# Kernel optimization log

Hardware: AMD Instinct MI355X
Metric: run time of the kernel (lower is better)

Reference implementation:

```python
import jax, jax.numpy as jnp
import numpy as np

BLOCK = 64
EPS = 1e-6
N_HEADS = 16


def _rope(t, cos, sin):
    # t: (B,S,H,hd); cos/sin: (S, hd//2) -> broadcast (1,S,1,hd//2)
    B, S, H, hd = t.shape
    tr = t.reshape(B, S, H, hd // 2, 2)
    t0, t1 = tr[..., 0], tr[..., 1]
    c = cos[None, :, None, :]
    s = sin[None, :, None, :]
    o0 = t0 * c - t1 * s
    o1 = t0 * s + t1 * c
    return jnp.stack([o0, o1], axis=-1).reshape(B, S, H, hd)


def setup_inputs() -> dict:
    key = jax.random.key(0)
    ks = jax.random.split(key, 6)
    B, S, D = 1, 2048, 2048
    hd = D // N_HEADS
    x = jax.random.normal(ks[0], (B, S, D), dtype=jnp.float32)
    # rotary table: theta_i = 10000^(-2i/hd)
    inv_freq = 1.0 / (10000.0 ** (jnp.arange(0, hd, 2, dtype=jnp.float32) / hd))
    t = jnp.arange(S, dtype=jnp.float32)
    freqs = jnp.outer(t, inv_freq)  # (S, hd//2)
    freqs_cos = jnp.cos(freqs)
    freqs_sin = jnp.sin(freqs)
    std = 0.02
    Wq = jax.random.normal(ks[1], (D, D), dtype=jnp.float32) * std
    Wk = jax.random.normal(ks[2], (D, D), dtype=jnp.float32) * std
    Wv = jax.random.normal(ks[3], (D, D), dtype=jnp.float32) * std
    Wo = jax.random.normal(ks[4], (D, D), dtype=jnp.float32) * std
    mask = jnp.ones((1, 1), dtype=bool)  # non-None mask => no masking in original code
    return {"x": x, "freqs_cos": freqs_cos, "freqs_sin": freqs_sin,
            "Wq": Wq, "Wk": Wk, "Wv": Wv, "Wo": Wo, "mask": mask}


def reference(x, freqs_cos, freqs_sin, Wq, Wk, Wv, Wo, mask):
    B, S, D = x.shape
    H = N_HEADS
    hd = D // H
    scale = hd ** -0.5
    nb = S // BLOCK

    q = (x @ Wq.T).reshape(B, S, H, hd)
    k = (x @ Wk.T).reshape(B, S, H, hd)
    v = (x @ Wv.T).reshape(B, S, H, hd)
    q = _rope(q, freqs_cos, freqs_sin)
    k = _rope(k, freqs_cos, freqs_sin)

    # block views: (B, nb, BLOCK, H, hd)
    qb = q.reshape(B, nb, BLOCK, H, hd)
    kb = k.reshape(B, nb, BLOCK, H, hd)
    vb = v.reshape(B, nb, BLOCK, H, hd)

    # per-(i,j) block scores: (B, nb_i, nb_j, H, BLOCK_q, BLOCK_k)
    s = jnp.einsum('binhd,bjmhd->bijhnm', qb, kb) * scale
    # NOTE: original module (mask is not None path) applies NO causal mask and
    # uses the per-block local max (no running-max rescale) -- reproduced exactly.
    m = jnp.max(s, axis=-1, keepdims=True)
    p = jnp.exp(s - m)
    # denominator: sum of per-block row sums over all j blocks -> (B, nb, H, BLOCK)
    L = p.sum(axis=-1).sum(axis=2)
    # numerator: sum over j blocks of p @ v -> (B, nb, BLOCK, H, hd)
    O = jnp.einsum('bijhnm,bjmhd->binhd', p, vb).reshape(B, S, H, hd)
    Lr = L.transpose(0, 1, 3, 2).reshape(B, S, H, 1)  # (B,S,H,1)
    O = O / (Lr + EPS)
    return O.reshape(B, S, D) @ Wo.T
```

## Files before the change

kernel.cpp:

```cpp
#include <hip/hip_runtime.h>
#include <hip/hip_bf16.h>
#include <math.h>

#define SEQ 2048
#define DM  2048
#define NH  16
#define HD  128
#define SCALE 0.08838834764831845f

typedef __bf16 bf16_t;
typedef __bf16 bf16x8 __attribute__((ext_vector_type(8)));
typedef __bf16 bf16x4 __attribute__((ext_vector_type(4)));
typedef float  f32x4  __attribute__((ext_vector_type(4)));
typedef int    i32x4  __attribute__((ext_vector_type(4)));

typedef const __attribute__((address_space(1))) void* gas_ptr;
typedef __attribute__((address_space(3))) void* las_ptr;

__device__ __forceinline__ void gload_lds16(const void* g, void* l) {
    __builtin_amdgcn_global_load_lds((gas_ptr)g, (las_ptr)l, 16, 0, 0);
}

__device__ __forceinline__ f32x4 mfma_bf16(bf16x8 a, bf16x8 b, f32x4 c) {
    return __builtin_amdgcn_mfma_f32_16x16x32_bf16(a, b, c, 0, 0, 0);
}

__device__ __forceinline__ unsigned cvtpk_bf16(float lo, float hi) {
    unsigned d;
    asm("v_cvt_pk_bf16_f32 %0, %1, %2" : "=v"(d) : "v"(lo), "v"(hi));
    return d;
}

__device__ __forceinline__ bf16x8 read_frag64(const bf16_t* lds, int row, int k) {
    int chunk = (k >> 3) ^ (row & 7);
    return *(const bf16x8*)(lds + row * 64 + chunk * 8);
}
__device__ __forceinline__ bf16x8 read_frag128(const bf16_t* lds, int row, int k) {
    int chunk = k >> 3;
    chunk = (chunk & 8) | ((chunk ^ row) & 7);
    return *(const bf16x8*)(lds + row * 128 + chunk * 8);
}
__device__ __forceinline__ bf16x8 read_slab(const bf16_t* sl, int row, int g) {
    int j = g ^ ((row >> 1) & 3);
    return *(const bf16x8*)(sl + row * 32 + j * 8);
}

__global__ __launch_bounds__(256) void cvt5(
    const float* __restrict__ s0, const float* __restrict__ s1,
    const float* __restrict__ s2, const float* __restrict__ s3,
    const float* __restrict__ s4,
    bf16_t* __restrict__ d0, bf16_t* __restrict__ d1, bf16_t* __restrict__ d2,
    bf16_t* __restrict__ d3, bf16_t* __restrict__ d4)
{
    int which = blockIdx.y;
    const float* s; bf16_t* d;
    switch (which) {
        case 0: s = s0; d = d0; break;
        case 1: s = s1; d = d1; break;
        case 2: s = s2; d = d2; break;
        case 3: s = s3; d = d3; break;
        default: s = s4; d = d4; break;
    }
    size_t idx = ((size_t)blockIdx.x * 256 + threadIdx.x) * 4;
    float4 v = *(const float4*)(s + idx);
    bf16x4 o = { (bf16_t)v.x, (bf16_t)v.y, (bf16_t)v.z, (bf16_t)v.w };
    *(bf16x4*)(d + idx) = o;
}

#define BARX() asm volatile("s_barrier" ::: "memory")
#define VMW8 asm volatile("s_waitcnt vmcnt(8)" ::: "memory")
#define VMW4 asm volatile("s_waitcnt vmcnt(4)" ::: "memory")
#define VMW0 asm volatile("s_waitcnt vmcnt(0)" ::: "memory")
#define NOGATE

__global__ __launch_bounds__(512, 2) void qkv_pipe(
    const bf16_t* __restrict__ A,
    const bf16_t* __restrict__ B0, const bf16_t* __restrict__ B1,
    const bf16_t* __restrict__ B2,
    bf16_t* __restrict__ Oq, bf16_t* __restrict__ Ok, bf16_t* __restrict__ Ov,
    const float* __restrict__ fcos, const float* __restrict__ fsin)
{
    __shared__ bf16_t lds[65536];

    const int tid = threadIdx.x;
    const int lane = tid & 63;
    const int w = tid >> 6;
    const int wm = w >> 2;
    const int wn = w & 3;
    const int g4 = lane >> 4, r15 = lane & 15;

    const int bm = blockIdx.y;
    const int bny = blockIdx.x;
    const int sel = bny >> 3;
    const int bnl = bny & 7;
    const bf16_t* Bp = (sel == 0) ? B0 : (sel == 1) ? B1 : B2;

    const size_t arow0 = (size_t)bm * 256;
    const size_t brow0 = (size_t)bnl * 256;

    const int row0 = tid >> 2;
    const int kj0  = (tid & 3) ^ ((row0 >> 1) & 3);
    const bf16_t* pA = A  + (arow0 + row0) * DM + kj0 * 8;
    const bf16_t* pB = Bp + (brow0 + row0) * DM + kj0 * 8;
    char* ldsb = (char*)lds;
    const int off0 = tid * 16;
    const int off1 = 8192 + tid * 16;

    #define STAGE_HT(S) do { if ((S) < 128) {                                   \
        const int T_ = (S) >> 2, a_ = (S) & 3;                                  \
        const int ko_ = T_ * 64 + ((a_ >> 1) << 5);                             \
        char* dst_ = ldsb + (((T_ & 1) << 16) | ((a_ & 1) << 15) | ((a_ >> 1) << 14)); \
        const bf16_t* s0_ = (a_ & 1) ? pB : pA;                                 \
        gload_lds16(s0_ + ko_, dst_ + off0);                                    \
        gload_lds16(s0_ + 128 * DM + ko_, dst_ + off1);                         \
    } } while (0)

    const bf16_t* b0A0 = lds;
    const bf16_t* b0A1 = lds + 8192;
    const bf16_t* b0B0 = lds + 16384;
    const bf16_t* b0B1 = lds + 24576;
    const bf16_t* b1A0 = lds + 32768;
    const bf16_t* b1A1 = lds + 40960;
    const bf16_t* b1B0 = lds + 49152;
    const bf16_t* b1B1 = lds + 57344;

    f32x4 acc[8][4] = {};

    #define PHASE(ASL, BSL, MH, SIDX, GATE, READB)                              \
    {                                                                           \
        _Pragma("unroll")                                                       \
        for (int m = 0; m < 4; ++m)                                             \
            af[m] = read_slab((ASL), wm * 128 + (MH) * 64 + m * 16 + r15, g4);  \
        if (READB) {                                                            \
            _Pragma("unroll")                                                   \
            for (int n = 0; n < 4; ++n)                                         \
                bfr[n] = read_slab((BSL), wn * 64 + n * 16 + r15, g4);          \
        }                                                                       \
        STAGE_HT(SIDX);                                                         \
        GATE;                                                                   \
        BARX();                                                                 \
        __builtin_amdgcn_s_setprio(1);                                          \
        _Pragma("unroll")                                                       \
        for (int m = 0; m < 4; ++m)                                             \
            _Pragma("unroll")                                                   \
            for (int n = 0; n < 4; ++n)                                         \
                acc[(MH) * 4 + m][n] = mfma_bf16(af[m], bfr[n], acc[(MH) * 4 + m][n]); \
        __builtin_amdgcn_s_setprio(0);                                          \
        BARX();                                                                 \
    }

    STAGE_HT(0); STAGE_HT(1); STAGE_HT(2); STAGE_HT(3); STAGE_HT(4); STAGE_HT(5);
    VMW8;
    BARX();

    for (int i = 0; i < 15; ++i) {
        const int s0 = 6 + i * 8;
        bf16x8 af[4], bfr[4];
        PHASE(b0A0, b0B0, 0, s0 + 0, NOGATE, 1)
        PHASE(b0A0, b0B0, 1, s0 + 1, VMW8,   0)
        PHASE(b0A1, b0B1, 0, s0 + 2, NOGATE, 1)
        PHASE(b0A1, b0B1, 1, s0 + 3, VMW8,   0)
        PHASE(b1A0, b1B0, 0, s0 + 4, NOGATE, 1)
        PHASE(b1A0, b1B0, 1, s0 + 5, VMW8,   0)
        PHASE(b1A1, b1B1, 0, s0 + 6, NOGATE, 1)
        PHASE(b1A1, b1B1, 1, s0 + 7, VMW8,   0)
    }
    {
        const int s0 = 6 + 15 * 8;
        bf16x8 af[4], bfr[4];
        PHASE(b0A0, b0B0, 0, s0 + 0, NOGATE, 1)
        PHASE(b0A0, b0B0, 1, s0 + 1, VMW8,   0)
        PHASE(b0A1, b0B1, 0, s0 + 2, NOGATE, 1)
        PHASE(b0A1, b0B1, 1, s0 + 3, VMW4,   0)
        PHASE(b1A0, b1B0, 0, s0 + 4, NOGATE, 1)
        PHASE(b1A0, b1B0, 1, s0 + 5, VMW0,   0)
        PHASE(b1A1, b1B1, 0, s0 + 6, NOGATE, 1)
        PHASE(b1A1, b1B1, 1, s0 + 7, NOGATE, 0)
    }
    #undef PHASE
    #undef STAGE_HT

    const int r0 = bm * 256 + wm * 128;
    const int c0 = bnl * 256 + wn * 64;

    if (sel == 2) {
        #pragma unroll
        for (int m = 0; m < 8; ++m) {
            int rowb = r0 + m * 16 + g4 * 4;
            #pragma unroll
            for (int n = 0; n < 4; ++n) {
                int col = c0 + n * 16 + r15;
                bf16x4 pk = { (bf16_t)acc[m][n][0], (bf16_t)acc[m][n][1],
                              (bf16_t)acc[m][n][2], (bf16_t)acc[m][n][3] };
                *(bf16x4*)&Ov[(size_t)col * SEQ + rowb] = pk;
            }
        }
    } else {
        bf16_t* dst = (sel == 0) ? Oq : Ok;
        #pragma unroll
        for (int m = 0; m < 8; ++m) {
            int rowb = r0 + m * 16 + g4 * 4;
            #pragma unroll
            for (int n = 0; n < 4; ++n) {
                int col = c0 + n * 16 + r15;
                int f = (col & (HD - 1)) >> 1;
                float sgn = (col & 1) ? 1.0f : -1.0f;
                #pragma unroll
                for (int r = 0; r < 4; ++r) {
                    float mine = acc[m][n][r];
                    float other = __shfl_xor(mine, 1);
                    float cc = fcos[(rowb + r) * (HD / 2) + f];
                    float ss = fsin[(rowb + r) * (HD / 2) + f];
                    float o = mine * cc + sgn * other * ss;
                    dst[(size_t)(rowb + r) * DM + col] = (bf16_t)o;
                }
            }
        }
    }
}

__global__ __launch_bounds__(256) void gemm_fin(
    const bf16_t* __restrict__ A, const bf16_t* __restrict__ B0,
    float* __restrict__ Of)
{
    __shared__ bf16_t lA[128 * 64];
    __shared__ bf16_t lB[64 * 64];

    const int tid = threadIdx.x;
    const int lane = tid & 63;
    const int w = tid >> 6;
    const int wm = w >> 1, wn = w & 1;
    const int g = lane >> 4, r15 = lane & 15;

    const int bm = blockIdx.x;
    const int bn = blockIdx.y;

    f32x4 acc[4][2] = {};

    const size_t arow0 = (size_t)bm * 128;
    const size_t brow0 = (size_t)bn * 64;

    for (int kt = 0; kt < DM / 64; ++kt) {
        const int k0 = kt * 64;
        #pragma unroll
        for (int i = 0; i < 4; ++i) {
            int c = i * 256 + tid;
            int row = c >> 3;
            int ck = (c ^ row) & 7;
            const bf16_t* ga = A + (arow0 + row) * DM + k0 + ck * 8;
            gload_lds16(ga, (char*)lA + (i * 256 + w * 64) * 16);
        }
        #pragma unroll
        for (int i = 0; i < 2; ++i) {
            int c = i * 256 + tid;
            int row = c >> 3;
            int ck = (c ^ row) & 7;
            const bf16_t* gb = B0 + (brow0 + row) * DM + k0 + ck * 8;
            gload_lds16(gb, (char*)lB + (i * 256 + w * 64) * 16);
        }
        __syncthreads();
        #pragma unroll
        for (int kk = 0; kk < 2; ++kk) {
            bf16x8 af[4], bfr[2];
            #pragma unroll
            for (int m = 0; m < 4; ++m)
                af[m] = read_frag64(lA, wm * 64 + m * 16 + r15, kk * 32 + g * 8);
            #pragma unroll
            for (int n = 0; n < 2; ++n)
                bfr[n] = read_frag64(lB, wn * 32 + n * 16 + r15, kk * 32 + g * 8);
            #pragma unroll
            for (int m = 0; m < 4; ++m)
                #pragma unroll
                for (int n = 0; n < 2; ++n)
                    acc[m][n] = mfma_bf16(af[m], bfr[n], acc[m][n]);
        }
        __syncthreads();
    }

    const int r0 = bm * 128 + wm * 64;
    const int c0 = bn * 64 + wn * 32;
    #pragma unroll
    for (int m = 0; m < 4; ++m) {
        int rowb = r0 + m * 16 + g * 4;
        #pragma unroll
        for (int n = 0; n < 2; ++n) {
            int col = c0 + n * 16 + r15;
            #pragma unroll
            for (int r = 0; r < 4; ++r)
                Of[(size_t)(rowb + r) * DM + col] = acc[m][n][r];
        }
    }
}

__global__ __launch_bounds__(512, 2) void attn_k6(
    const bf16_t* __restrict__ Q, const bf16_t* __restrict__ Kb,
    const bf16_t* __restrict__ Vt, bf16_t* __restrict__ Op,
    float* __restrict__ Lp)
{
    __shared__ bf16_t lk[2 * 64 * 128];
    __shared__ bf16_t lv[2 * 128 * 64];

    const int tid = threadIdx.x;
    const int lane = tid & 63;
    const int w = tid >> 6;
    const int g = lane >> 4, r15 = lane & 15;
    const int qb = blockIdx.x;
    const int h = blockIdx.y;
    const int sp = blockIdx.z;
    const int j0 = sp * 8;

    const int lo = g & 1, hb = g >> 1;
    const int e_src = (lo << 5) + r15;
    const int o_src = e_src + 16;
    const int sA = hb ? o_src : e_src;
    const int sB = hb ? e_src : o_src;

    bf16x8 qf[2][4];
    #pragma unroll
    for (int u = 0; u < 2; ++u) {
        const bf16_t* qrow = Q + (size_t)(qb * 256 + w * 32 + u * 16 + r15) * DM + h * HD + g * 8;
        #pragma unroll
        for (int ks = 0; ks < 4; ++ks)
            qf[u][ks] = *(const bf16x8*)(qrow + ks * 32);
    }

    f32x4 oacc[2][8] = {};
    float Lsum[2] = {0.f, 0.f};

    #define STAGE_KV(JJ, BUF)                                                     \
    {                                                                             \
        _Pragma("unroll")                                                         \
        for (int i = 0; i < 2; ++i) {                                             \
            int c = i * 512 + tid;                                                \
            int row = c >> 4, ckl = c & 15;                                       \
            int ck = (ckl & 8) | ((ckl ^ row) & 7);                               \
            const bf16_t* gk = Kb + (size_t)((JJ) * 64 + row) * DM + h * HD + ck * 8; \
            gload_lds16(gk, (char*)lk + (BUF) * 16384 + (i * 512 + w * 64) * 16); \
        }                                                                         \
        _Pragma("unroll")                                                         \
        for (int i = 0; i < 2; ++i) {                                             \
            int c = i * 512 + tid;                                                \
            int row = c >> 3;                                                     \
            int ck = (c ^ row) & 7;                                               \
            const bf16_t* gv = Vt + (size_t)(h * HD + row) * SEQ + (JJ) * 64 + ck * 8; \
            gload_lds16(gv, (char*)lv + (BUF) * 16384 + (i * 512 + w * 64) * 16); \
        }                                                                         \
    }

    STAGE_KV(j0, 0);
    asm volatile("s_waitcnt vmcnt(0)" ::: "memory");
    __builtin_amdgcn_s_barrier();

    for (int jj = 0; jj < 8; ++jj) {
        const int cur = jj & 1;
        const bf16_t* lkc = lk + cur * 8192;
        const bf16_t* lvc = lv + cur * 8192;
        if (jj < 7) STAGE_KV(j0 + jj + 1, cur ^ 1);

        f32x4 sacc[2][4] = {};
        __builtin_amdgcn_s_setprio(1);
        #pragma unroll
        for (int ks = 0; ks < 4; ++ks) {
            #pragma unroll
            for (int n = 0; n < 4; ++n) {
                bf16x8 kf = read_frag128(lkc, n * 16 + r15, ks * 32 + g * 8);
                sacc[0][n] = mfma_bf16(kf, qf[0][ks], sacc[0][n]);
                sacc[1][n] = mfma_bf16(kf, qf[1][ks], sacc[1][n]);
            }
        }
        __builtin_amdgcn_s_setprio(0);

        bf16x8 pa0[2], pa1[2];
        #pragma unroll
        for (int u = 0; u < 2; ++u) {
            float mx0 = fmaxf(fmaxf(sacc[u][0][0], sacc[u][0][1]), fmaxf(sacc[u][0][2], sacc[u][0][3]));
            float mx1 = fmaxf(fmaxf(sacc[u][1][0], sacc[u][1][1]), fmaxf(sacc[u][1][2], sacc[u][1][3]));
            float mx2 = fmaxf(fmaxf(sacc[u][2][0], sacc[u][2][1]), fmaxf(sacc[u][2][2], sacc[u][2][3]));
            float mx3 = fmaxf(fmaxf(sacc[u][3][0], sacc[u][3][1]), fmaxf(sacc[u][3][2], sacc[u][3][3]));
            float mx = fmaxf(fmaxf(mx0, mx1), fmaxf(mx2, mx3));
            mx = fmaxf(mx, __shfl_xor(mx, 16));
            mx = fmaxf(mx, __shfl_xor(mx, 32));

            float p[4][4];
            float ls = 0.f;
            #pragma unroll
            for (int n = 0; n < 4; ++n)
                #pragma unroll
                for (int r = 0; r < 4; ++r) {
                    float pv = __expf((sacc[u][n][r] - mx) * SCALE);
                    p[n][r] = pv;
                    ls += pv;
                }
            Lsum[u] += ls;

            unsigned D00 = cvtpk_bf16(p[0][0], p[0][1]), D01 = cvtpk_bf16(p[0][2], p[0][3]);
            unsigned D10 = cvtpk_bf16(p[1][0], p[1][1]), D11 = cvtpk_bf16(p[1][2], p[1][3]);
            unsigned D20 = cvtpk_bf16(p[2][0], p[2][1]), D21 = cvtpk_bf16(p[2][2], p[2][3]);
            unsigned D30 = cvtpk_bf16(p[3][0], p[3][1]), D31 = cvtpk_bf16(p[3][2], p[3][3]);

            unsigned r0 = __shfl((int)(lo ? D10 : D00), sA);
            unsigned r1 = __shfl((int)(lo ? D11 : D01), sA);
            unsigned r2 = __shfl((int)(lo ? D00 : D10), sB);
            unsigned r3 = __shfl((int)(lo ? D01 : D11), sB);
            unsigned r4 = __shfl((int)(lo ? D30 : D20), sA);
            unsigned r5 = __shfl((int)(lo ? D31 : D21), sA);
            unsigned r6 = __shfl((int)(lo ? D20 : D30), sB);
            unsigned r7 = __shfl((int)(lo ? D21 : D31), sB);
            i32x4 w0, w1;
            w0[0] = (int)(hb ? r2 : r0);  w0[1] = (int)(hb ? r3 : r1);
            w0[2] = (int)(hb ? r0 : r2);  w0[3] = (int)(hb ? r1 : r3);
            w1[0] = (int)(hb ? r6 : r4);  w1[1] = (int)(hb ? r7 : r5);
            w1[2] = (int)(hb ? r4 : r6);  w1[3] = (int)(hb ? r5 : r7);
            pa0[u] = __builtin_bit_cast(bf16x8, w0);
            pa1[u] = __builtin_bit_cast(bf16x8, w1);
        }

        __builtin_amdgcn_s_setprio(1);
        #pragma unroll
        for (int n = 0; n < 8; ++n) {
            bf16x8 bv0 = read_frag64(lvc, n * 16 + r15, g * 8);
            oacc[0][n] = mfma_bf16(pa0[0], bv0, oacc[0][n]);
            oacc[1][n] = mfma_bf16(pa0[1], bv0, oacc[1][n]);
            bf16x8 bv1 = read_frag64(lvc, n * 16 + r15, 32 + g * 8);
            oacc[0][n] = mfma_bf16(pa1[0], bv1, oacc[0][n]);
            oacc[1][n] = mfma_bf16(pa1[1], bv1, oacc[1][n]);
        }
        __builtin_amdgcn_s_setprio(0);

        asm volatile("s_waitcnt vmcnt(0)" ::: "memory");
        __builtin_amdgcn_s_barrier();
    }

    #pragma unroll
    for (int u = 0; u < 2; ++u) {
        float L = Lsum[u];
        L += __shfl_xor(L, 16);
        L += __shfl_xor(L, 32);
        int qrow = qb * 256 + w * 32 + u * 16;
        if (g == 0)
            Lp[((size_t)sp * NH + h) * SEQ + qrow + r15] = L;

        #pragma unroll
        for (int n = 0; n < 8; ++n) {
            int col = h * HD + n * 16 + r15;
            int rowb = qrow + g * 4;
            #pragma unroll
            for (int r = 0; r < 4; ++r)
                Op[(size_t)sp * SEQ * DM + (size_t)(rowb + r) * DM + col] = (bf16_t)oacc[u][n][r];
        }
    }
}

__global__ __launch_bounds__(256) void attn_cmb(
    const bf16_t* __restrict__ Op, const float* __restrict__ Lp,
    bf16_t* __restrict__ Ob)
{
    const int row = blockIdx.x;
    const int c0 = threadIdx.x * 8;
    const int h = c0 >> 7;

    float L = 1e-6f;
    #pragma unroll
    for (int s = 0; s < 4; ++s)
        L += Lp[((size_t)s * NH + h) * SEQ + row];

    float acc[8] = {};
    #pragma unroll
    for (int s = 0; s < 4; ++s) {
        bf16x8 v = *(const bf16x8*)(Op + (size_t)s * SEQ * DM + (size_t)row * DM + c0);
        #pragma unroll
        for (int j = 0; j < 8; ++j)
            acc[j] += (float)v[j];
    }
    float inv = 1.0f / L;
    bf16x8 o;
    #pragma unroll
    for (int j = 0; j < 8; ++j)
        o[j] = (bf16_t)(acc[j] * inv);
    *(bf16x8*)(Ob + (size_t)row * DM + c0) = o;
}

extern "C" void kernel_launch(void* const* d_in, const int* in_sizes, int n_in,
                              void* d_out, int out_size, void* d_ws, size_t ws_size,
                              hipStream_t stream)
{
    const float* x    = (const float*)d_in[0];
    const float* fcos = (const float*)d_in[1];
    const float* fsin = (const float*)d_in[2];
    const float* Wq   = (const float*)d_in[3];
    const float* Wk   = (const float*)d_in[4];
    const float* Wv   = (const float*)d_in[5];
    const float* Wo   = (const float*)d_in[6];
    float* out = (float*)d_out;

    const size_t NE = (size_t)DM * SEQ;
    bf16_t* ws  = (bf16_t*)d_ws;
    bf16_t* xb  = ws;
    bf16_t* wqb = ws + 1 * NE;
    bf16_t* wkb = ws + 2 * NE;
    bf16_t* wvb = ws + 3 * NE;
    bf16_t* wob = ws + 4 * NE;
    bf16_t* qr  = ws + 5 * NE;
    bf16_t* kr  = ws + 6 * NE;
    bf16_t* vt  = ws + 7 * NE;
    bf16_t* ob  = ws + 8 * NE;
    bf16_t* op  = ws;
    float*  lp  = (float*)(ws + 9 * NE);

    hipLaunchKernelGGL(cvt5, dim3(4096, 5), dim3(256), 0, stream,
                       x, Wq, Wk, Wv, Wo, xb, wqb, wkb, wvb, wob);

    hipLaunchKernelGGL(qkv_pipe, dim3(24, 8), dim3(512), 0, stream,
                       xb, wqb, wkb, wvb, qr, kr, vt, fcos, fsin);

    hipLaunchKernelGGL(attn_k6, dim3(8, 16, 4), dim3(512), 0, stream,
                       qr, kr, vt, op, lp);

    hipLaunchKernelGGL(attn_cmb, dim3(2048), dim3(256), 0, stream,
                       op, lp, ob);

    hipLaunchKernelGGL(gemm_fin, dim3(16, 32), dim3(256), 0, stream,
                       ob, wob, out);
}
```

Before: 176.3 us.

## Merge QKV GEMM phases into wider steps and reshape attention grid

The QKV GEMM main loop now loads all eight A fragments and four B fragments per slab and issues 32 MFMAs per barrier pair, staging two tiles per phase. This halves the number of barriers and phase switches, at the cost of more live registers. Separately, the attention kernel moves to 256-thread blocks covering 128 query rows, with each block handling 16 key blocks over a 2-way split instead of 4. The combine kernel correspondingly sums only two partials, cutting partial-output traffic but giving each block a longer serial loop.

```diff
diff --git a/kernel.cpp b/kernel.cpp
--- a/kernel.cpp
+++ b/kernel.cpp
@@ -126,25 +126,24 @@
 
     f32x4 acc[8][4] = {};
 
-    #define PHASE(ASL, BSL, MH, SIDX, GATE, READB)                              \
+    #define PHASE2(ASL, BSL, S1, S2, GATE)                                      \
     {                                                                           \
+        GATE;                                                                   \
         _Pragma("unroll")                                                       \
-        for (int m = 0; m < 4; ++m)                                             \
-            af[m] = read_slab((ASL), wm * 128 + (MH) * 64 + m * 16 + r15, g4);  \
-        if (READB) {                                                            \
-            _Pragma("unroll")                                                   \
-            for (int n = 0; n < 4; ++n)                                         \
-                bfr[n] = read_slab((BSL), wn * 64 + n * 16 + r15, g4);          \
-        }                                                                       \
-        STAGE_HT(SIDX);                                                         \
-        GATE;                                                                   \
+        for (int k = 0; k < 8; ++k)                                             \
+            af[k] = read_slab((ASL), wm * 128 + k * 16 + r15, g4);              \
+        _Pragma("unroll")                                                       \
+        for (int n = 0; n < 4; ++n)                                             \
+            bfr[n] = read_slab((BSL), wn * 64 + n * 16 + r15, g4);              \
+        STAGE_HT(S1);                                                           \
+        STAGE_HT(S2);                                                           \
         BARX();                                                                 \
         __builtin_amdgcn_s_setprio(1);                                          \
         _Pragma("unroll")                                                       \
-        for (int m = 0; m < 4; ++m)                                             \
+        for (int k = 0; k < 8; ++k)                                             \
             _Pragma("unroll")                                                   \
             for (int n = 0; n < 4; ++n)                                         \
-                acc[(MH) * 4 + m][n] = mfma_bf16(af[m], bfr[n], acc[(MH) * 4 + m][n]); \
+                acc[k][n] = mfma_bf16(af[k], bfr[n], acc[k][n]);                \
         __builtin_amdgcn_s_setprio(0);                                          \
         BARX();                                                                 \
     }
@@ -155,29 +154,20 @@
 
     for (int i = 0; i < 15; ++i) {
         const int s0 = 6 + i * 8;
-        bf16x8 af[4], bfr[4];
-        PHASE(b0A0, b0B0, 0, s0 + 0, NOGATE, 1)
-        PHASE(b0A0, b0B0, 1, s0 + 1, VMW8,   0)
-        PHASE(b0A1, b0B1, 0, s0 + 2, NOGATE, 1)
-        PHASE(b0A1, b0B1, 1, s0 + 3, VMW8,   0)
-        PHASE(b1A0, b1B0, 0, s0 + 4, NOGATE, 1)
-        PHASE(b1A0, b1B0, 1, s0 + 5, VMW8,   0)
-        PHASE(b1A1, b1B1, 0, s0 + 6, NOGATE, 1)
-        PHASE(b1A1, b1B1, 1, s0 + 7, VMW8,   0)
+        bf16x8 af[8], bfr[4];
+        PHASE2(b0A0, b0B0, s0 + 0, s0 + 1, VMW8)
+        PHASE2(b0A1, b0B1, s0 + 2, s0 + 3, VMW8)
+        PHASE2(b1A0, b1B0, s0 + 4, s0 + 5, VMW8)
+        PHASE2(b1A1, b1B1, s0 + 6, s0 + 7, VMW8)
     }
     {
-        const int s0 = 6 + 15 * 8;
-        bf16x8 af[4], bfr[4];
-        PHASE(b0A0, b0B0, 0, s0 + 0, NOGATE, 1)
-        PHASE(b0A0, b0B0, 1, s0 + 1, VMW8,   0)
-        PHASE(b0A1, b0B1, 0, s0 + 2, NOGATE, 1)
-        PHASE(b0A1, b0B1, 1, s0 + 3, VMW4,   0)
-        PHASE(b1A0, b1B0, 0, s0 + 4, NOGATE, 1)
-        PHASE(b1A0, b1B0, 1, s0 + 5, VMW0,   0)
-        PHASE(b1A1, b1B1, 0, s0 + 6, NOGATE, 1)
-        PHASE(b1A1, b1B1, 1, s0 + 7, NOGATE, 0)
-    }
-    #undef PHASE
+        bf16x8 af[8], bfr[4];
+        PHASE2(b0A0, b0B0, 126, 127, VMW8)
+        PHASE2(b0A1, b0B1, 200, 200, VMW8)
+        PHASE2(b1A0, b1B0, 200, 200, VMW4)
+        PHASE2(b1A1, b1B1, 200, 200, VMW0)
+    }
+    #undef PHASE2
     #undef STAGE_HT
 
     const int r0 = bm * 256 + wm * 128;
@@ -292,7 +282,7 @@
     }
 }
 
-__global__ __launch_bounds__(512, 2) void attn_k6(
+__global__ __launch_bounds__(256, 2) void attn_k6(
     const bf16_t* __restrict__ Q, const bf16_t* __restrict__ Kb,
     const bf16_t* __restrict__ Vt, bf16_t* __restrict__ Op,
     float* __restrict__ Lp)
@@ -307,7 +297,7 @@
     const int qb = blockIdx.x;
     const int h = blockIdx.y;
     const int sp = blockIdx.z;
-    const int j0 = sp * 8;
+    const int j0 = sp * 16;
 
     const int lo = g & 1, hb = g >> 1;
     const int e_src = (lo << 5) + r15;
@@ -318,7 +308,7 @@
     bf16x8 qf[2][4];
     #pragma unroll
     for (int u = 0; u < 2; ++u) {
-        const bf16_t* qrow = Q + (size_t)(qb * 256 + w * 32 + u * 16 + r15) * DM + h * HD + g * 8;
+        const bf16_t* qrow = Q + (size_t)(qb * 128 + w * 32 + u * 16 + r15) * DM + h * HD + g * 8;
         #pragma unroll
         for (int ks = 0; ks < 4; ++ks)
             qf[u][ks] = *(const bf16x8*)(qrow + ks * 32);
@@ -330,20 +320,20 @@
     #define STAGE_KV(JJ, BUF)                                                     \
     {                                                                             \
         _Pragma("unroll")                                                         \
-        for (int i = 0; i < 2; ++i) {                                             \
-            int c = i * 512 + tid;                                                \
+        for (int i = 0; i < 4; ++i) {                                             \
+            int c = i * 256 + tid;                                                \
             int row = c >> 4, ckl = c & 15;                                       \
             int ck = (ckl & 8) | ((ckl ^ row) & 7);                               \
             const bf16_t* gk = Kb + (size_t)((JJ) * 64 + row) * DM + h * HD + ck * 8; \
-            gload_lds16(gk, (char*)lk + (BUF) * 16384 + (i * 512 + w * 64) * 16); \
+            gload_lds16(gk, (char*)lk + (BUF) * 16384 + (i * 256 + w * 64) * 16); \
         }                                                                         \
         _Pragma("unroll")                                                         \
-        for (int i = 0; i < 2; ++i) {                                             \
-            int c = i * 512 + tid;                                                \
+        for (int i = 0; i < 4; ++i) {                                             \
+            int c = i * 256 + tid;                                                \
             int row = c >> 3;                                                     \
             int ck = (c ^ row) & 7;                                               \
             const bf16_t* gv = Vt + (size_t)(h * HD + row) * SEQ + (JJ) * 64 + ck * 8; \
-            gload_lds16(gv, (char*)lv + (BUF) * 16384 + (i * 512 + w * 64) * 16); \
+            gload_lds16(gv, (char*)lv + (BUF) * 16384 + (i * 256 + w * 64) * 16); \
         }                                                                         \
     }
 
@@ -351,11 +341,11 @@
     asm volatile("s_waitcnt vmcnt(0)" ::: "memory");
     __builtin_amdgcn_s_barrier();
 
-    for (int jj = 0; jj < 8; ++jj) {
+    for (int jj = 0; jj < 16; ++jj) {
         const int cur = jj & 1;
         const bf16_t* lkc = lk + cur * 8192;
         const bf16_t* lvc = lv + cur * 8192;
-        if (jj < 7) STAGE_KV(j0 + jj + 1, cur ^ 1);
+        if (jj < 15) STAGE_KV(j0 + jj + 1, cur ^ 1);
 
         f32x4 sacc[2][4] = {};
         __builtin_amdgcn_s_setprio(1);
@@ -436,7 +426,7 @@
         float L = Lsum[u];
         L += __shfl_xor(L, 16);
         L += __shfl_xor(L, 32);
-        int qrow = qb * 256 + w * 32 + u * 16;
+        int qrow = qb * 128 + w * 32 + u * 16;
         if (g == 0)
             Lp[((size_t)sp * NH + h) * SEQ + qrow + r15] = L;
 
@@ -461,12 +451,12 @@
 
     float L = 1e-6f;
     #pragma unroll
-    for (int s = 0; s < 4; ++s)
+    for (int s = 0; s < 2; ++s)
         L += Lp[((size_t)s * NH + h) * SEQ + row];
 
     float acc[8] = {};
     #pragma unroll
-    for (int s = 0; s < 4; ++s) {
+    for (int s = 0; s < 2; ++s) {
         bf16x8 v = *(const bf16x8*)(Op + (size_t)s * SEQ * DM + (size_t)row * DM + c0);
         #pragma unroll
         for (int j = 0; j < 8; ++j)
@@ -513,7 +503,7 @@
     hipLaunchKernelGGL(qkv_pipe, dim3(24, 8), dim3(512), 0, stream,
                        xb, wqb, wkb, wvb, qr, kr, vt, fcos, fsin);
 
-    hipLaunchKernelGGL(attn_k6, dim3(8, 16, 4), dim3(512), 0, stream,
+    hipLaunchKernelGGL(attn_k6, dim3(16, 16, 2), dim3(256), 0, stream,
                        qr, kr, vt, op, lp);
 
     hipLaunchKernelGGL(attn_cmb, dim3(2048), dim3(256), 0, stream,
```

After: 166.1 us (median of 3 runs). -5.8%, faster.
